# Performance work log

Measured on AMD Instinct MI355X. Metric: run time of the kernel, lower is better.

Reference implementation:

```python
import jax, jax.numpy as jnp
import numpy as np

NUM_COLS = 8      # MyTopoAgent.num_columns
NUM_SELECTED = 4  # MyTopoAgent.num_selected


def _gatv2(x, src, tgt, Wl, bl, Wr, br, att, bias, n):
    """PyG GATv2Conv (share_weights=False, concat=True, negative_slope=0.2).
    x: [n, Din]; src/tgt: [E] (self loops already appended); att: [H, C]."""
    H, C = att.shape
    xl = (x @ Wl + bl).reshape(n, H, C)   # lin_l(x) -> source transform
    xr = (x @ Wr + br).reshape(n, H, C)   # lin_r(x) -> target transform
    # e_ij = att . leaky_relu(xl[j] + xr[i])  per head
    e = jnp.einsum('ehc,hc->eh', jax.nn.leaky_relu(xl[src] + xr[tgt], 0.2), att)  # [E, H]
    # segment softmax over edges sharing a target node (stable via segment max)
    m = jax.lax.stop_gradient(jax.ops.segment_max(e, tgt, num_segments=n))
    ex = jnp.exp(e - m[tgt])
    denom = jax.ops.segment_sum(ex, tgt, num_segments=n)
    alpha = ex / (denom[tgt] + 1e-16)
    out = jax.ops.segment_sum(xl[src] * alpha[..., None], tgt, num_segments=n)  # [n, H, C]
    return out.reshape(n, H * C) + bias


def setup_inputs() -> dict:
    key = jax.random.key(0)
    B, N, D, Hd, Ch, E = 4, 10000, 128, 128, 7, 640000
    M = B * N
    ks = iter(jax.random.split(key, 40))
    nx = lambda shape: jax.random.normal(next(ks), shape, dtype=jnp.float32) * 0.05
    inp = {}
    inp['x'] = jax.random.normal(next(ks), (B, N, D), dtype=jnp.float32)
    inp['edge_index'] = jax.random.randint(next(ks), (2, E), 0, M)
    inp['gumbel_u'] = jax.random.uniform(next(ks), (B, NUM_COLS, Ch), dtype=jnp.float32,
                                         minval=1e-6, maxval=1.0 - 1e-6)
    # actor gat1(D->Hd), actor gat2(Hd->Ch), critic gat1(D->Hd), critic gat2(Hd->Hd); heads=1
    for pre, di, do in (('a1', D, Hd), ('a2', Hd, Ch), ('c1', D, Hd), ('c2', Hd, Hd)):
        inp[pre + '_Wl'] = nx((di, do))
        inp[pre + '_bl'] = jnp.zeros((do,), jnp.float32)
        inp[pre + '_Wr'] = nx((di, do))
        inp[pre + '_br'] = jnp.zeros((do,), jnp.float32)
        inp[pre + '_att'] = nx((1, do))
        inp[pre + '_b'] = jnp.zeros((do,), jnp.float32)
    inp['fc_W'] = nx((Hd, 1))
    inp['fc_b'] = jnp.zeros((1,), jnp.float32)
    return inp


def reference(x, edge_index, gumbel_u,
              a1_Wl, a1_bl, a1_Wr, a1_br, a1_att, a1_b,
              a2_Wl, a2_bl, a2_Wr, a2_br, a2_att, a2_b,
              c1_Wl, c1_bl, c1_Wr, c1_br, c1_att, c1_b,
              c2_Wl, c2_bl, c2_Wr, c2_br, c2_att, c2_b,
              fc_W, fc_b):
    B, N, D = x.shape
    M = B * N
    xf = x.reshape(M, D)
    loops = jnp.arange(M, dtype=edge_index.dtype)  # PyG add_self_loops
    src = jnp.concatenate([edge_index[0], loops])
    tgt = jnp.concatenate([edge_index[1], loops])
    # ---- actor: GATv2 -> leaky_relu(0.01) -> GATv2 -> softmax ----
    h = _gatv2(xf, src, tgt, a1_Wl, a1_bl, a1_Wr, a1_br, a1_att, a1_b, M)
    h = jax.nn.leaky_relu(h, 0.01)
    logits = _gatv2(h, src, tgt, a2_Wl, a2_bl, a2_Wr, a2_br, a2_att, a2_b, M).reshape(B, N, -1)
    probs = jax.nn.softmax(logits, axis=-1)  # [B, N, 7]
    # multinomial(k=4, no replacement) per column via Gumbel top-k
    g = -jnp.log(-jnp.log(gumbel_u))                       # [B, 8, 7]
    scores = jnp.log(probs[:, :NUM_COLS, :]) + g
    _, action = jax.lax.top_k(scores, NUM_SELECTED)        # [B, 8, 4]
    # torch gather(dim=1): sel[b,i,j] = probs[b, action[b,i,j], j]
    sel = probs[jnp.arange(B)[:, None, None], action, jnp.arange(NUM_SELECTED)[None, None, :]]
    # ---- critic: GATv2 -> leaky_relu(0.01) -> GATv2 -> Linear ----
    hc = _gatv2(xf, src, tgt, c1_Wl, c1_bl, c1_Wr, c1_br, c1_att, c1_b, M)
    hc = jax.nn.leaky_relu(hc, 0.01)
    hc = _gatv2(hc, src, tgt, c2_Wl, c2_bl, c2_Wr, c2_br, c2_att, c2_b, M).reshape(B, N, -1)
    value = hc @ fc_W + fc_b  # [B, N, 1]
    return action, sel, value
```

## Files before the change

kernel.cpp:

```cpp
#include <hip/hip_runtime.h>
#include <math.h>


typedef __attribute__((ext_vector_type(8))) short bf16x8;
typedef __attribute__((ext_vector_type(4))) float f32x4;

__device__ __forceinline__ float wave_reduce_sum(float v){
  #pragma unroll
  for (int o = 32; o > 0; o >>= 1) v += __shfl_xor(v, o);
  return v;
}
__device__ __forceinline__ unsigned short f2bf(float f){
  unsigned int u = __float_as_uint(f);
  u += 0x7FFFu + ((u >> 16) & 1u);
  return (unsigned short)(u >> 16);
}
__device__ __forceinline__ void unpack2(unsigned int u, float& a, float& b){
  a = __uint_as_float(u << 16);
  b = __uint_as_float(u & 0xffff0000u);
}

__global__ void k_init(int* __restrict__ p, int nz,
                       const float* __restrict__ W1l, const float* __restrict__ W1r,
                       const float* __restrict__ W2l, const float* __restrict__ W2r,
                       unsigned short* __restrict__ Wt1, unsigned short* __restrict__ Wt2){
  int i = blockIdx.x * blockDim.x + threadIdx.x;
  if (i < nz){
    p[i] = 0;
  } else {
    int r = i - nz;
    if (r < 65536){
      int which = r >> 15;
      int lin = r & 32767;
      const float* Wl = which ? W2l : W1l;
      const float* Wr = which ? W2r : W1r;
      unsigned short* Wt = which ? Wt2 : Wt1;
      int n = lin >> 7, k = lin & 127;
      float v = (n < 128) ? Wl[(size_t)k * 128 + n] : Wr[(size_t)k * 128 + (n - 128)];
      Wt[lin] = f2bf(v);
    }
  }
}

__global__ void k_scatter(const int* __restrict__ ei, int E,
                          int* __restrict__ cnt, int* __restrict__ bucket){
  int e = blockIdx.x * blockDim.x + threadIdx.x;
  if (e >= E) return;
  int s = ei[e], t = ei[E + e];
  int pos = atomicAdd(&cnt[t], 1);
  if (pos < 64) bucket[(size_t)t * 64 + pos] = s;
}

__device__ __forceinline__ void dev_mark1(
    const int* __restrict__ cnt, const int* __restrict__ bucket,
    int* __restrict__ flag1, int* __restrict__ list1, int* __restrict__ n1, int N){
  int p = threadIdx.x;
  if (p >= 32) return;
  int node = (p >> 3) * N + (p & 7);
  if (atomicExch(&flag1[node], 1) == 0) list1[atomicAdd(n1, 1)] = node;
  int deg = min(cnt[node], 64);
  const int* crow = bucket + (size_t)node * 64;
  for (int j = 0; j < deg; ++j){
    int s = crow[j];
    if (atomicExch(&flag1[s], 1) == 0) list1[atomicAdd(n1, 1)] = s;
  }
}
__device__ __forceinline__ void dev_mark2(
    int vbid, int nblk,
    const int* __restrict__ cnt, const int* __restrict__ bucket,
    const int* __restrict__ list1, const int* __restrict__ n1,
    int* __restrict__ flag2, int* __restrict__ list2, int* __restrict__ n2){
  int n = *n1;
  for (int i = vbid * blockDim.x + threadIdx.x; i < n; i += nblk * blockDim.x){
    int node = list1[i];
    if (atomicExch(&flag2[node], 1) == 0) list2[atomicAdd(n2, 1)] = node;
    int deg = min(cnt[node], 64);
    const int* crow = bucket + (size_t)node * 64;
    for (int j = 0; j < deg; ++j){
      int s = crow[j];
      if (atomicExch(&flag2[s], 1) == 0) list2[atomicAdd(n2, 1)] = s;
    }
  }
}

__device__ __forceinline__ void dev_gemm_dual(
    int bid, const float* __restrict__ A,
    const float* __restrict__ Wl, const float* __restrict__ Wr,
    const float* __restrict__ blv, const float* __restrict__ brv,
    float* __restrict__ XL1, float* __restrict__ XR1,
    const int* __restrict__ list1, const int* __restrict__ list2,
    const int* __restrict__ nn,
    float (*As)[17], float (*Ws)[64]){
  const float* W; const float* bias; float* Out; const int* rows; int n;
  int colBase, bx, nbx;
  if (bid < 384){
    W = Wl; bias = blv; Out = XL1; rows = list2; n = nn[1];
    colBase = (bid / 192) * 64; bx = bid % 192; nbx = 192;
  } else {
    int rem = bid - 384;
    W = Wr; bias = brv; Out = XR1; rows = list1; n = nn[0];
    colBase = (rem / 64) * 64; bx = rem % 64; nbx = 64;
  }
  int tid = threadIdx.x;
  int tx = tid & 15, ty = tid >> 4;
  int ar = tid >> 2, ac = (tid & 3) << 2;
  int kr = tid >> 4, nc = (tid & 15) << 2;
  for (int base = bx * 64; base < n; base += nbx * 64){
    float acc[4][4] = {};
    int arow = rows[min(base + ar, n - 1)];
    for (int k0 = 0; k0 < 128; k0 += 16){
      float4 av = *(const float4*)(A + (size_t)arow * 128 + k0 + ac);
      As[ar][ac + 0] = av.x; As[ar][ac + 1] = av.y;
      As[ar][ac + 2] = av.z; As[ar][ac + 3] = av.w;
      float4 wv = *(const float4*)(W + (size_t)(k0 + kr) * 128 + colBase + nc);
      *(float4*)&Ws[kr][nc] = wv;
      __syncthreads();
      #pragma unroll
      for (int kk = 0; kk < 16; ++kk){
        float a0 = As[ty * 4 + 0][kk];
        float a1 = As[ty * 4 + 1][kk];
        float a2 = As[ty * 4 + 2][kk];
        float a3 = As[ty * 4 + 3][kk];
        float4 b = *(const float4*)&Ws[kk][tx * 4];
        acc[0][0] += a0 * b.x; acc[0][1] += a0 * b.y; acc[0][2] += a0 * b.z; acc[0][3] += a0 * b.w;
        acc[1][0] += a1 * b.x; acc[1][1] += a1 * b.y; acc[1][2] += a1 * b.z; acc[1][3] += a1 * b.w;
        acc[2][0] += a2 * b.x; acc[2][1] += a2 * b.y; acc[2][2] += a2 * b.z; acc[2][3] += a2 * b.w;
        acc[3][0] += a3 * b.x; acc[3][1] += a3 * b.y; acc[3][2] += a3 * b.z; acc[3][3] += a3 * b.w;
      }
      __syncthreads();
    }
    int cN = colBase + tx * 4;
    float4 bb = *(const float4*)(bias + cN);
    #pragma unroll
    for (int i = 0; i < 4; ++i){
      int r = rows[min(base + ty * 4 + i, n - 1)];
      float4 o;
      o.x = acc[i][0] + bb.x; o.y = acc[i][1] + bb.y;
      o.z = acc[i][2] + bb.z; o.w = acc[i][3] + bb.w;
      *(float4*)(Out + (size_t)r * 128 + cN) = o;
    }
  }
}

template<bool CVT>
__device__ __forceinline__ void dev_gemm_mfma(
    int rblk, const void* __restrict__ Av, const unsigned short* __restrict__ Wt,
    const float* __restrict__ bl, const float* __restrict__ br,
    unsigned short* __restrict__ XL, unsigned short* __restrict__ XR){
  int w = threadIdx.x >> 6, lane = threadIdx.x & 63;
  int l16 = lane & 15, kg = lane >> 4;
  int rBase = rblk * 64 + w * 16;
  f32x4 acc[16];
  #pragma unroll
  for (int i = 0; i < 16; ++i) acc[i] = (f32x4){0.f, 0.f, 0.f, 0.f};
  #pragma unroll
  for (int ks = 0; ks < 4; ++ks){
    bf16x8 a;
    if constexpr (CVT){
      const float* A = (const float*)Av;
      const float* ap = A + (size_t)(rBase + l16) * 128 + ks * 32 + kg * 8;
      float4 f0 = *(const float4*)ap;
      float4 f1 = *(const float4*)(ap + 4);
      union { bf16x8 v; unsigned short s[8]; } u;
      u.s[0] = f2bf(f0.x); u.s[1] = f2bf(f0.y); u.s[2] = f2bf(f0.z); u.s[3] = f2bf(f0.w);
      u.s[4] = f2bf(f1.x); u.s[5] = f2bf(f1.y); u.s[6] = f2bf(f1.z); u.s[7] = f2bf(f1.w);
      a = u.v;
    } else {
      a = *(const bf16x8*)((const unsigned short*)Av + (size_t)(rBase + l16) * 128 + ks * 32 + kg * 8);
    }
    #pragma unroll
    for (int ct = 0; ct < 16; ++ct){
      bf16x8 wv = *(const bf16x8*)(Wt + (size_t)(ct * 16 + l16) * 128 + ks * 32 + kg * 8);
      acc[ct] = __builtin_amdgcn_mfma_f32_16x16x32_bf16(wv, a, acc[ct], 0, 0, 0);
    }
  }
  int row = rBase + l16;
  #pragma unroll
  for (int ct = 0; ct < 16; ++ct){
    int col = ct * 16 + kg * 4;
    const float* bp = (col < 128) ? (bl + col) : (br + (col - 128));
    float4 bb = *(const float4*)bp;
    unsigned int p0 = (unsigned int)f2bf(acc[ct][0] + bb.x) |
                      ((unsigned int)f2bf(acc[ct][1] + bb.y) << 16);
    unsigned int p1 = (unsigned int)f2bf(acc[ct][2] + bb.z) |
                      ((unsigned int)f2bf(acc[ct][3] + bb.w) << 16);
    unsigned short* dst = (col < 128) ? (XL + (size_t)row * 128 + col)
                                      : (XR + (size_t)row * 128 + (col - 128));
    uint2 pk; pk.x = p0; pk.y = p1;
    *(uint2*)dst = pk;
  }
}

template<int MODE>
__device__ __forceinline__ void dev_gather16(
    int gid, int l,
    const unsigned short* __restrict__ XL, const unsigned short* __restrict__ XR,
    const int* __restrict__ cnt, const int* __restrict__ bucket,
    const float* __restrict__ att, const float* __restrict__ bias,
    const float* __restrict__ fcW, const float* __restrict__ fcb,
    void* __restrict__ outp){
  uint4 xu = *(const uint4*)(XR + (size_t)gid * 128 + l * 8);
  float xr[8];
  unpack2(xu.x, xr[0], xr[1]); unpack2(xu.y, xr[2], xr[3]);
  unpack2(xu.z, xr[4], xr[5]); unpack2(xu.w, xr[6], xr[7]);
  float at[8];
  {
    float4 a0 = *(const float4*)(att + l * 8);
    float4 a1 = *(const float4*)(att + l * 8 + 4);
    at[0] = a0.x; at[1] = a0.y; at[2] = a0.z; at[3] = a0.w;
    at[4] = a1.x; at[5] = a1.y; at[6] = a1.z; at[7] = a1.w;
  }
  int deg = min(cnt[gid], 64);
  const int* __restrict__ crow = bucket + (size_t)gid * 64;
  float m = -INFINITY, den = 0.f;
  float acc[8] = {0.f, 0.f, 0.f, 0.f, 0.f, 0.f, 0.f, 0.f};

  auto proc = [&](uint4 u){
    float xl[8];
    unpack2(u.x, xl[0], xl[1]); unpack2(u.y, xl[2], xl[3]);
    unpack2(u.z, xl[4], xl[5]); unpack2(u.w, xl[6], xl[7]);
    float e = 0.f;
    #pragma unroll
    for (int c = 0; c < 8; ++c){
      float v = xl[c] + xr[c];
      v = fmaxf(v, 0.2f * v);
      e = fmaf(v, at[c], e);
    }
    e += __shfl_xor(e, 1, 16);
    e += __shfl_xor(e, 2, 16);
    e += __shfl_xor(e, 4, 16);
    e += __shfl_xor(e, 8, 16);
    if (e > m){
      float sc = __expf(m - e);
      den *= sc;
      #pragma unroll
      for (int c = 0; c < 8; ++c) acc[c] *= sc;
      m = e;
    }
    float p = __expf(e - m);
    den += p;
    #pragma unroll
    for (int c = 0; c < 8; ++c) acc[c] = fmaf(p, xl[c], acc[c]);
  };

  proc(*(const uint4*)(XL + (size_t)gid * 128 + l * 8));

  int nq = deg >> 2;
  int j = 0;
  if (nq > 0){
    uint4 r0, r1, r2, r3;
    {
      int s0 = crow[0], s1 = crow[1], s2 = crow[2], s3 = crow[3];
      r0 = *(const uint4*)(XL + (size_t)s0 * 128 + l * 8);
      r1 = *(const uint4*)(XL + (size_t)s1 * 128 + l * 8);
      r2 = *(const uint4*)(XL + (size_t)s2 * 128 + l * 8);
      r3 = *(const uint4*)(XL + (size_t)s3 * 128 + l * 8);
    }
    for (int q = 1;; ++q){
      bool more = (q < nq);
      uint4 n0, n1, n2, n3;
      if (more){
        int b4 = q * 4;
        int t0 = crow[b4 + 0], t1 = crow[b4 + 1], t2 = crow[b4 + 2], t3 = crow[b4 + 3];
        n0 = *(const uint4*)(XL + (size_t)t0 * 128 + l * 8);
        n1 = *(const uint4*)(XL + (size_t)t1 * 128 + l * 8);
        n2 = *(const uint4*)(XL + (size_t)t2 * 128 + l * 8);
        n3 = *(const uint4*)(XL + (size_t)t3 * 128 + l * 8);
      }
      proc(r0); proc(r1); proc(r2); proc(r3);
      if (!more) break;
      r0 = n0; r1 = n1; r2 = n2; r3 = n3;
    }
    j = nq * 4;
  }
  for (; j < deg; ++j){
    int s = crow[j];
    proc(*(const uint4*)(XL + (size_t)s * 128 + l * 8));
  }

  float r = 1.f / (den + 1e-16f);
  float4 b0 = *(const float4*)(bias + l * 8);
  float4 b1 = *(const float4*)(bias + l * 8 + 4);
  float o[8];
  o[0] = acc[0] * r + b0.x; o[1] = acc[1] * r + b0.y;
  o[2] = acc[2] * r + b0.z; o[3] = acc[3] * r + b0.w;
  o[4] = acc[4] * r + b1.x; o[5] = acc[5] * r + b1.y;
  o[6] = acc[6] * r + b1.z; o[7] = acc[7] * r + b1.w;
  if (MODE == 0){
    #pragma unroll
    for (int c = 0; c < 8; ++c) o[c] = o[c] > 0.f ? o[c] : 0.01f * o[c];
    uint4 pk;
    pk.x = (unsigned int)f2bf(o[0]) | ((unsigned int)f2bf(o[1]) << 16);
    pk.y = (unsigned int)f2bf(o[2]) | ((unsigned int)f2bf(o[3]) << 16);
    pk.z = (unsigned int)f2bf(o[4]) | ((unsigned int)f2bf(o[5]) << 16);
    pk.w = (unsigned int)f2bf(o[6]) | ((unsigned int)f2bf(o[7]) << 16);
    *(uint4*)((unsigned short*)outp + (size_t)gid * 128 + l * 8) = pk;
  } else {
    float4 w0 = *(const float4*)(fcW + l * 8);
    float4 w1 = *(const float4*)(fcW + l * 8 + 4);
    float pv = o[0] * w0.x + o[1] * w0.y + o[2] * w0.z + o[3] * w0.w +
               o[4] * w1.x + o[5] * w1.y + o[6] * w1.z + o[7] * w1.w;
    pv += __shfl_xor(pv, 1, 16);
    pv += __shfl_xor(pv, 2, 16);
    pv += __shfl_xor(pv, 4, 16);
    pv += __shfl_xor(pv, 8, 16);
    if (l == 0) ((float*)outp)[gid] = pv + fcb[0];
  }
}

__device__ __forceinline__ void dev_a1_fused(
    int vbid,
    const float* __restrict__ XL, const float* __restrict__ XR,
    const int* __restrict__ cnt, const int* __restrict__ bucket,
    const float* __restrict__ att, const float* __restrict__ bias,
    const float* __restrict__ Wl7, const float* __restrict__ Wr7,
    const float* __restrict__ bl7, const float* __restrict__ br7,
    float* __restrict__ XL2, float* __restrict__ XR2,
    const int* __restrict__ list, const int* __restrict__ n_dev){
  int n = *n_dev;
  int lane = threadIdx.x & 63;
  const int wstride = (256 * 256) >> 6;
  for (int i = (vbid * 256 + (int)threadIdx.x) >> 6; i < n; i += wstride){
    int wid = list[i];
    float2 xr = ((const float2*)(XR + (size_t)wid * 128))[lane];
    float2 at = ((const float2*)att)[lane];
    int deg = min(cnt[wid], 64);
    const int* crow = bucket + (size_t)wid * 64;
    float m = -INFINITY, den = 0.f, acc0 = 0.f, acc1 = 0.f;
    for (int j = -1; j < deg; ++j){
      int s = (j < 0) ? wid : crow[j];
      float2 xl = ((const float2*)(XL + (size_t)s * 128))[lane];
      float v0 = xl.x + xr.x, v1 = xl.y + xr.y;
      v0 = v0 > 0.f ? v0 : 0.2f * v0;
      v1 = v1 > 0.f ? v1 : 0.2f * v1;
      float e = wave_reduce_sum(v0 * at.x + v1 * at.y);
      float mn = fmaxf(m, e);
      float sc = __expf(m - mn);
      float p  = __expf(e - mn);
      den  = den  * sc + p;
      acc0 = acc0 * sc + p * xl.x;
      acc1 = acc1 * sc + p * xl.y;
      m = mn;
    }
    float r = 1.f / (den + 1e-16f);
    float2 bs = ((const float2*)bias)[lane];
    float o0 = acc0 * r + bs.x;
    float o1 = acc1 * r + bs.y;
    o0 = o0 > 0.f ? o0 : 0.01f * o0;
    o1 = o1 > 0.f ? o1 : 0.01f * o1;
    #pragma unroll
    for (int c = 0; c < 7; ++c){
      float wl0 = Wl7[(size_t)(2 * lane) * 7 + c];
      float wl1 = Wl7[(size_t)(2 * lane + 1) * 7 + c];
      float wr0 = Wr7[(size_t)(2 * lane) * 7 + c];
      float wr1 = Wr7[(size_t)(2 * lane + 1) * 7 + c];
      float dl = wave_reduce_sum(o0 * wl0 + o1 * wl1);
      float dr = wave_reduce_sum(o0 * wr0 + o1 * wr1);
      if (lane == 0){
        XL2[(size_t)wid * 8 + c] = dl + bl7[c];
        XR2[(size_t)wid * 8 + c] = dr + br7[c];
      }
    }
  }
}

__global__ __launch_bounds__(256) void k_L3(
    const float* __restrict__ x, const unsigned short* __restrict__ Wt1,
    const float* __restrict__ c1_bl, const float* __restrict__ c1_br,
    unsigned short* __restrict__ XLb, unsigned short* __restrict__ XRb, int nMfma,
    const int* __restrict__ cnt, const int* __restrict__ bucket,
    int* __restrict__ flag1, int* __restrict__ list1, int* __restrict__ n1, int N){
  int bid = blockIdx.x;
  if (bid < nMfma){
    dev_gemm_mfma<true>(bid, x, Wt1, c1_bl, c1_br, XLb, XRb);
  } else {
    dev_mark1(cnt, bucket, flag1, list1, n1, N);
  }
}

__global__ __launch_bounds__(256) void k_L4(
    const int* __restrict__ cnt, const int* __restrict__ bucket,
    const int* __restrict__ list1, const int* __restrict__ n1,
    int* __restrict__ flag2, int* __restrict__ list2, int* __restrict__ n2,
    const unsigned short* __restrict__ XLb, const unsigned short* __restrict__ XRb,
    const float* __restrict__ c1_att, const float* __restrict__ c1_b,
    unsigned short* __restrict__ Hb, int M){
  int bid = blockIdx.x;
  if (bid < 64){
    dev_mark2(bid, 64, cnt, bucket, list1, n1, flag2, list2, n2);
  } else {
    int gbid = bid - 64;
    int gid = (gbid * 256 + (int)threadIdx.x) >> 4;
    int l = threadIdx.x & 15;
    if (gid < M)
      dev_gather16<0>(gid, l, XLb, XRb, cnt, bucket, c1_att, c1_b,
                      nullptr, nullptr, (void*)Hb);
  }
}

__global__ __launch_bounds__(256) void k_L5(
    const float* __restrict__ x,
    const float* __restrict__ a1_Wl, const float* __restrict__ a1_Wr,
    const float* __restrict__ a1_bl, const float* __restrict__ a1_br,
    float* __restrict__ XL1, float* __restrict__ XR1,
    const int* __restrict__ list1, const int* __restrict__ list2,
    const int* __restrict__ nn,
    const unsigned short* __restrict__ Hb, const unsigned short* __restrict__ Wt2,
    const float* __restrict__ c2_bl, const float* __restrict__ c2_br,
    unsigned short* __restrict__ XLb, unsigned short* __restrict__ XRb){
  __shared__ float As[64][17];
  __shared__ float Ws[16][64];
  int bid = blockIdx.x;
  if (bid < 512){
    dev_gemm_dual(bid, x, a1_Wl, a1_Wr, a1_bl, a1_br, XL1, XR1, list1, list2, nn, As, Ws);
  } else {
    dev_gemm_mfma<false>(bid - 512, Hb, Wt2, c2_bl, c2_br, XLb, XRb);
  }
}

__global__ __launch_bounds__(256) void k_L6(
    const float* __restrict__ XL1, const float* __restrict__ XR1,
    const int* __restrict__ cnt, const int* __restrict__ bucket,
    const float* __restrict__ a1_att, const float* __restrict__ a1_b,
    const float* __restrict__ Wl7, const float* __restrict__ Wr7,
    const float* __restrict__ bl7, const float* __restrict__ br7,
    float* __restrict__ XL2, float* __restrict__ XR2,
    const int* __restrict__ list1, const int* __restrict__ n1,
    const unsigned short* __restrict__ XLb, const unsigned short* __restrict__ XRb,
    const float* __restrict__ c2_att, const float* __restrict__ c2_b,
    const float* __restrict__ fcW, const float* __restrict__ fcb,
    float* __restrict__ out_value, int M){
  int bid = blockIdx.x;
  if (bid < 256){
    dev_a1_fused(bid, XL1, XR1, cnt, bucket, a1_att, a1_b,
                 Wl7, Wr7, bl7, br7, XL2, XR2, list1, n1);
  } else {
    int gbid = bid - 256;
    int gid = (gbid * 256 + (int)threadIdx.x) >> 4;
    int l = threadIdx.x & 15;
    if (gid < M)
      dev_gather16<1>(gid, l, XLb, XRb, cnt, bucket, c2_att, c2_b,
                      fcW, fcb, (void*)out_value);
  }
}

__global__ __launch_bounds__(256) void k_a2head(
    const float* __restrict__ XL2, const float* __restrict__ XR2,
    const int* __restrict__ cnt, const int* __restrict__ bucket,
    const float* __restrict__ att, const float* __restrict__ bias,
    const float* __restrict__ gu,
    float* __restrict__ out_action, float* __restrict__ out_sel, int N){
  __shared__ float pr[32][8];
  int g = threadIdx.x >> 3, c = threadIdx.x & 7;
  int node = (g >> 3) * N + (g & 7);
  float xr = (c < 7) ? XR2[(size_t)node * 8 + c] : 0.f;
  float at = (c < 7) ? att[c] : 0.f;
  int deg = min(cnt[node], 64);
  const int* crow = bucket + (size_t)node * 64;
  float m = -INFINITY, den = 0.f, acc = 0.f;
  for (int j = -1; j < deg; ++j){
    int s = (j < 0) ? node : crow[j];
    float xl = (c < 7) ? XL2[(size_t)s * 8 + c] : 0.f;
    float v = xl + xr;
    v = fmaxf(v, 0.2f * v);
    float e = v * at;
    e += __shfl_xor(e, 1, 8);
    e += __shfl_xor(e, 2, 8);
    e += __shfl_xor(e, 4, 8);
    if (e > m){
      float sc = __expf(m - e);
      den *= sc; acc *= sc; m = e;
    }
    float p = __expf(e - m);
    den += p;
    acc = fmaf(p, xl, acc);
  }
  float lg = acc / (den + 1e-16f) + ((c < 7) ? bias[c] : 0.f);
  float lgv = (c < 7) ? lg : -INFINITY;
  float mx = lgv;
  mx = fmaxf(mx, __shfl_xor(mx, 1, 8));
  mx = fmaxf(mx, __shfl_xor(mx, 2, 8));
  mx = fmaxf(mx, __shfl_xor(mx, 4, 8));
  float ex = (c < 7) ? expf(lgv - mx) : 0.f;
  float sm = ex;
  sm += __shfl_xor(sm, 1, 8);
  sm += __shfl_xor(sm, 2, 8);
  sm += __shfl_xor(sm, 4, 8);
  pr[g][c] = ex / sm;
  __syncthreads();
  int t = threadIdx.x;
  if (t < 32){
    int b = t >> 3;
    float sc[7];
    #pragma unroll
    for (int cc = 0; cc < 7; ++cc){
      float u = gu[t * 7 + cc];
      float gn = -logf(-logf(u));
      sc[cc] = logf(pr[t][cc]) + gn;
    }
    #pragma unroll
    for (int k = 0; k < 4; ++k){
      float best = -INFINITY; int bi = 0;
      #pragma unroll
      for (int cc = 0; cc < 7; ++cc) if (sc[cc] > best){ best = sc[cc]; bi = cc; }
      sc[bi] = -INFINITY;
      out_action[t * 4 + k] = (float)bi;
      out_sel[t * 4 + k] = pr[b * 8 + bi][k];
    }
  }
}

extern "C" void kernel_launch(void* const* d_in, const int* in_sizes, int n_in,
                              void* d_out, int out_size, void* d_ws, size_t ws_size,
                              hipStream_t stream){
  const float* x  = (const float*)d_in[0];
  const int*   ei = (const int*)d_in[1];
  const float* gu = (const float*)d_in[2];
  const float* a1_Wl = (const float*)d_in[3],  *a1_bl = (const float*)d_in[4];
  const float* a1_Wr = (const float*)d_in[5],  *a1_br = (const float*)d_in[6];
  const float* a1_att= (const float*)d_in[7],  *a1_b  = (const float*)d_in[8];
  const float* a2_Wl = (const float*)d_in[9],  *a2_bl = (const float*)d_in[10];
  const float* a2_Wr = (const float*)d_in[11], *a2_br = (const float*)d_in[12];
  const float* a2_att= (const float*)d_in[13], *a2_b  = (const float*)d_in[14];
  const float* c1_Wl = (const float*)d_in[15], *c1_bl = (const float*)d_in[16];
  const float* c1_Wr = (const float*)d_in[17], *c1_br = (const float*)d_in[18];
  const float* c1_att= (const float*)d_in[19], *c1_b  = (const float*)d_in[20];
  const float* c2_Wl = (const float*)d_in[21], *c2_bl = (const float*)d_in[22];
  const float* c2_Wr = (const float*)d_in[23], *c2_br = (const float*)d_in[24];
  const float* c2_att= (const float*)d_in[25], *c2_b  = (const float*)d_in[26];
  const float* fc_W  = (const float*)d_in[27], *fc_b  = (const float*)d_in[28];

  const int M = in_sizes[0] / 128;
  const int E = in_sizes[1] / 2;
  const int B = in_sizes[2] / 56;
  const int N = M / B;
  const int nw = B * 8;
  const int T = 256;

  char* ws = (char*)d_ws;
  size_t off = 0;
  auto alloc = [&](size_t bytes) -> void* {
    void* p = ws + off;
    off += (bytes + 255) & ~(size_t)255;
    return p;
  };
  int*   cnt    = (int*)alloc((size_t)(3 * M + 2) * 4);
  int*   flag1  = cnt + M;
  int*   flag2  = flag1 + M;
  int*   nn     = flag2 + M;
  int*   bucket = (int*)alloc((size_t)M * 64 * 4);
  int*   list1  = (int*)alloc((size_t)M * 4);
  int*   list2  = (int*)alloc((size_t)M * 4);
  float* XL2    = (float*)alloc((size_t)M * 8 * 4);
  float* XR2    = (float*)alloc((size_t)M * 8 * 4);
  unsigned short* Wt1 = (unsigned short*)alloc((size_t)256 * 128 * 2);
  unsigned short* Wt2 = (unsigned short*)alloc((size_t)256 * 128 * 2);
  float* XL1 = (float*)alloc((size_t)M * 128 * 4);
  float* XR1 = (float*)alloc((size_t)M * 128 * 4);
  unsigned short* XLb = (unsigned short*)alloc((size_t)M * 128 * 2);
  unsigned short* XRb = (unsigned short*)alloc((size_t)M * 128 * 2);
  unsigned short* Hb  = (unsigned short*)alloc((size_t)M * 128 * 2);
  (void)ws_size; (void)n_in; (void)out_size;

  float* out_action = (float*)d_out;
  float* out_sel    = out_action + (size_t)nw * 4;
  float* out_value  = out_sel + (size_t)nw * 4;

  const int G0 = (M * 16 + T - 1) / T;
  const int nMfma = M / 64;
  const int nz = 3 * M + 2;

  k_init<<<(nz + 65536 + T - 1) / T, T, 0, stream>>>(cnt, nz,
      c1_Wl, c1_Wr, c2_Wl, c2_Wr, Wt1, Wt2);
  k_scatter<<<(E + T - 1) / T, T, 0, stream>>>(ei, E, cnt, bucket);
  k_L3<<<nMfma + 1, T, 0, stream>>>(x, Wt1, c1_bl, c1_br, XLb, XRb, nMfma,
      cnt, bucket, flag1, list1, &nn[0], N);
  k_L4<<<64 + G0, T, 0, stream>>>(cnt, bucket, list1, &nn[0], flag2, list2, &nn[1],
      XLb, XRb, c1_att, c1_b, Hb, M);
  k_L5<<<512 + nMfma, T, 0, stream>>>(x, a1_Wl, a1_Wr, a1_bl, a1_br,
      XL1, XR1, list1, list2, nn, Hb, Wt2, c2_bl, c2_br, XLb, XRb);
  k_L6<<<256 + G0, T, 0, stream>>>(XL1, XR1, cnt, bucket, a1_att, a1_b,
      a2_Wl, a2_Wr, a2_bl, a2_br, XL2, XR2, list1, &nn[0],
      XLb, XRb, c2_att, c2_b, fc_W, fc_b, out_value, M);
  k_a2head<<<1, 256, 0, stream>>>(XL2, XR2, cnt, bucket, a2_att, a2_b, gu,
      out_action, out_sel, N);
}
```

Measured before the change: 207.6 us.

## Store edge buckets as 16-bit indices and fold the actor head into k_L6

```diff
diff --git a/kernel.cpp b/kernel.cpp
--- a/kernel.cpp
+++ b/kernel.cpp
@@ -43,23 +43,23 @@
 }
 
 __global__ void k_scatter(const int* __restrict__ ei, int E,
-                          int* __restrict__ cnt, int* __restrict__ bucket){
+                          int* __restrict__ cnt, unsigned short* __restrict__ bucket){
   int e = blockIdx.x * blockDim.x + threadIdx.x;
   if (e >= E) return;
   int s = ei[e], t = ei[E + e];
   int pos = atomicAdd(&cnt[t], 1);
-  if (pos < 64) bucket[(size_t)t * 64 + pos] = s;
+  if (pos < 64) bucket[(size_t)t * 64 + pos] = (unsigned short)s;
 }
 
 __device__ __forceinline__ void dev_mark1(
-    const int* __restrict__ cnt, const int* __restrict__ bucket,
+    const int* __restrict__ cnt, const unsigned short* __restrict__ bucket,
     int* __restrict__ flag1, int* __restrict__ list1, int* __restrict__ n1, int N){
   int p = threadIdx.x;
   if (p >= 32) return;
   int node = (p >> 3) * N + (p & 7);
   if (atomicExch(&flag1[node], 1) == 0) list1[atomicAdd(n1, 1)] = node;
   int deg = min(cnt[node], 64);
-  const int* crow = bucket + (size_t)node * 64;
+  const unsigned short* crow = bucket + (size_t)node * 64;
   for (int j = 0; j < deg; ++j){
     int s = crow[j];
     if (atomicExch(&flag1[s], 1) == 0) list1[atomicAdd(n1, 1)] = s;
@@ -67,7 +67,7 @@
 }
 __device__ __forceinline__ void dev_mark2(
     int vbid, int nblk,
-    const int* __restrict__ cnt, const int* __restrict__ bucket,
+    const int* __restrict__ cnt, const unsigned short* __restrict__ bucket,
     const int* __restrict__ list1, const int* __restrict__ n1,
     int* __restrict__ flag2, int* __restrict__ list2, int* __restrict__ n2){
   int n = *n1;
@@ -75,7 +75,7 @@
     int node = list1[i];
     if (atomicExch(&flag2[node], 1) == 0) list2[atomicAdd(n2, 1)] = node;
     int deg = min(cnt[node], 64);
-    const int* crow = bucket + (size_t)node * 64;
+    const unsigned short* crow = bucket + (size_t)node * 64;
     for (int j = 0; j < deg; ++j){
       int s = crow[j];
       if (atomicExch(&flag2[s], 1) == 0) list2[atomicAdd(n2, 1)] = s;
@@ -195,7 +195,7 @@
 __device__ __forceinline__ void dev_gather16(
     int gid, int l,
     const unsigned short* __restrict__ XL, const unsigned short* __restrict__ XR,
-    const int* __restrict__ cnt, const int* __restrict__ bucket,
+    const int* __restrict__ cnt, const unsigned short* __restrict__ bucket,
     const float* __restrict__ att, const float* __restrict__ bias,
     const float* __restrict__ fcW, const float* __restrict__ fcb,
     void* __restrict__ outp){
@@ -211,7 +211,7 @@
     at[4] = a1.x; at[5] = a1.y; at[6] = a1.z; at[7] = a1.w;
   }
   int deg = min(cnt[gid], 64);
-  const int* __restrict__ crow = bucket + (size_t)gid * 64;
+  const unsigned short* __restrict__ crow = bucket + (size_t)gid * 64;
   float m = -INFINITY, den = 0.f;
   float acc[8] = {0.f, 0.f, 0.f, 0.f, 0.f, 0.f, 0.f, 0.f};
 
@@ -311,7 +311,7 @@
 __device__ __forceinline__ void dev_a1_fused(
     int vbid,
     const float* __restrict__ XL, const float* __restrict__ XR,
-    const int* __restrict__ cnt, const int* __restrict__ bucket,
+    const int* __restrict__ cnt, const unsigned short* __restrict__ bucket,
     const float* __restrict__ att, const float* __restrict__ bias,
     const float* __restrict__ Wl7, const float* __restrict__ Wr7,
     const float* __restrict__ bl7, const float* __restrict__ br7,
@@ -325,7 +325,7 @@
     float2 xr = ((const float2*)(XR + (size_t)wid * 128))[lane];
     float2 at = ((const float2*)att)[lane];
     int deg = min(cnt[wid], 64);
-    const int* crow = bucket + (size_t)wid * 64;
+    const unsigned short* crow = bucket + (size_t)wid * 64;
     float m = -INFINITY, den = 0.f, acc0 = 0.f, acc1 = 0.f;
     for (int j = -1; j < deg; ++j){
       int s = (j < 0) ? wid : crow[j];
@@ -364,11 +364,77 @@
   }
 }
 
+__device__ __forceinline__ void dev_a2head(
+    float (*pr)[8],
+    const float* __restrict__ XL2, const float* __restrict__ XR2,
+    const int* __restrict__ cnt, const unsigned short* __restrict__ bucket,
+    const float* __restrict__ att, const float* __restrict__ bias,
+    const float* __restrict__ gu,
+    float* __restrict__ out_action, float* __restrict__ out_sel, int N){
+  int g = threadIdx.x >> 3, c = threadIdx.x & 7;
+  int node = (g >> 3) * N + (g & 7);
+  float xr = (c < 7) ? XR2[(size_t)node * 8 + c] : 0.f;
+  float at = (c < 7) ? att[c] : 0.f;
+  int deg = min(cnt[node], 64);
+  const unsigned short* crow = bucket + (size_t)node * 64;
+  float m = -INFINITY, den = 0.f, acc = 0.f;
+  for (int j = -1; j < deg; ++j){
+    int s = (j < 0) ? node : crow[j];
+    float xl = (c < 7) ? XL2[(size_t)s * 8 + c] : 0.f;
+    float v = xl + xr;
+    v = fmaxf(v, 0.2f * v);
+    float e = v * at;
+    e += __shfl_xor(e, 1, 8);
+    e += __shfl_xor(e, 2, 8);
+    e += __shfl_xor(e, 4, 8);
+    if (e > m){
+      float sc = __expf(m - e);
+      den *= sc; acc *= sc; m = e;
+    }
+    float p = __expf(e - m);
+    den += p;
+    acc = fmaf(p, xl, acc);
+  }
+  float lg = acc / (den + 1e-16f) + ((c < 7) ? bias[c] : 0.f);
+  float lgv = (c < 7) ? lg : -INFINITY;
+  float mx = lgv;
+  mx = fmaxf(mx, __shfl_xor(mx, 1, 8));
+  mx = fmaxf(mx, __shfl_xor(mx, 2, 8));
+  mx = fmaxf(mx, __shfl_xor(mx, 4, 8));
+  float ex = (c < 7) ? expf(lgv - mx) : 0.f;
+  float sm = ex;
+  sm += __shfl_xor(sm, 1, 8);
+  sm += __shfl_xor(sm, 2, 8);
+  sm += __shfl_xor(sm, 4, 8);
+  pr[g][c] = ex / sm;
+  __syncthreads();
+  int t = threadIdx.x;
+  if (t < 32){
+    int b = t >> 3;
+    float sc[7];
+    #pragma unroll
+    for (int cc = 0; cc < 7; ++cc){
+      float u = gu[t * 7 + cc];
+      float gn = -logf(-logf(u));
+      sc[cc] = logf(pr[t][cc]) + gn;
+    }
+    #pragma unroll
+    for (int k = 0; k < 4; ++k){
+      float best = -INFINITY; int bi = 0;
+      #pragma unroll
+      for (int cc = 0; cc < 7; ++cc) if (sc[cc] > best){ best = sc[cc]; bi = cc; }
+      sc[bi] = -INFINITY;
+      out_action[t * 4 + k] = (float)bi;
+      out_sel[t * 4 + k] = pr[b * 8 + bi][k];
+    }
+  }
+}
+
 __global__ __launch_bounds__(256) void k_L3(
     const float* __restrict__ x, const unsigned short* __restrict__ Wt1,
     const float* __restrict__ c1_bl, const float* __restrict__ c1_br,
     unsigned short* __restrict__ XLb, unsigned short* __restrict__ XRb, int nMfma,
-    const int* __restrict__ cnt, const int* __restrict__ bucket,
+    const int* __restrict__ cnt, const unsigned short* __restrict__ bucket,
     int* __restrict__ flag1, int* __restrict__ list1, int* __restrict__ n1, int N){
   int bid = blockIdx.x;
   if (bid < nMfma){
@@ -379,7 +445,7 @@
 }
 
 __global__ __launch_bounds__(256) void k_L4(
-    const int* __restrict__ cnt, const int* __restrict__ bucket,
+    const int* __restrict__ cnt, const unsigned short* __restrict__ bucket,
     const int* __restrict__ list1, const int* __restrict__ n1,
     int* __restrict__ flag2, int* __restrict__ list2, int* __restrict__ n2,
     const unsigned short* __restrict__ XLb, const unsigned short* __restrict__ XRb,
@@ -420,20 +486,38 @@
 
 __global__ __launch_bounds__(256) void k_L6(
     const float* __restrict__ XL1, const float* __restrict__ XR1,
-    const int* __restrict__ cnt, const int* __restrict__ bucket,
+    const int* __restrict__ cnt, const unsigned short* __restrict__ bucket,
     const float* __restrict__ a1_att, const float* __restrict__ a1_b,
     const float* __restrict__ Wl7, const float* __restrict__ Wr7,
     const float* __restrict__ bl7, const float* __restrict__ br7,
     float* __restrict__ XL2, float* __restrict__ XR2,
     const int* __restrict__ list1, const int* __restrict__ n1,
+    int* __restrict__ done,
+    const float* __restrict__ a2_att, const float* __restrict__ a2_b,
+    const float* __restrict__ gu,
+    float* __restrict__ out_action, float* __restrict__ out_sel, int N,
     const unsigned short* __restrict__ XLb, const unsigned short* __restrict__ XRb,
     const float* __restrict__ c2_att, const float* __restrict__ c2_b,
     const float* __restrict__ fcW, const float* __restrict__ fcb,
     float* __restrict__ out_value, int M){
+  __shared__ float pr[32][8];
+  __shared__ int isLast;
   int bid = blockIdx.x;
   if (bid < 256){
     dev_a1_fused(bid, XL1, XR1, cnt, bucket, a1_att, a1_b,
                  Wl7, Wr7, bl7, br7, XL2, XR2, list1, n1);
+    __syncthreads();
+    if (threadIdx.x == 0){
+      __threadfence();
+      int v = atomicAdd(done, 1);
+      isLast = (v == 255);
+    }
+    __syncthreads();
+    if (isLast){
+      __threadfence();
+      dev_a2head(pr, XL2, XR2, cnt, bucket, a2_att, a2_b, gu,
+                 out_action, out_sel, N);
+    }
   } else {
     int gbid = bid - 256;
     int gid = (gbid * 256 + (int)threadIdx.x) >> 4;
@@ -441,72 +525,6 @@
     if (gid < M)
       dev_gather16<1>(gid, l, XLb, XRb, cnt, bucket, c2_att, c2_b,
                       fcW, fcb, (void*)out_value);
-  }
-}
-
-__global__ __launch_bounds__(256) void k_a2head(
-    const float* __restrict__ XL2, const float* __restrict__ XR2,
-    const int* __restrict__ cnt, const int* __restrict__ bucket,
-    const float* __restrict__ att, const float* __restrict__ bias,
-    const float* __restrict__ gu,
-    float* __restrict__ out_action, float* __restrict__ out_sel, int N){
-  __shared__ float pr[32][8];
-  int g = threadIdx.x >> 3, c = threadIdx.x & 7;
-  int node = (g >> 3) * N + (g & 7);
-  float xr = (c < 7) ? XR2[(size_t)node * 8 + c] : 0.f;
-  float at = (c < 7) ? att[c] : 0.f;
-  int deg = min(cnt[node], 64);
-  const int* crow = bucket + (size_t)node * 64;
-  float m = -INFINITY, den = 0.f, acc = 0.f;
-  for (int j = -1; j < deg; ++j){
-    int s = (j < 0) ? node : crow[j];
-    float xl = (c < 7) ? XL2[(size_t)s * 8 + c] : 0.f;
-    float v = xl + xr;
-    v = fmaxf(v, 0.2f * v);
-    float e = v * at;
-    e += __shfl_xor(e, 1, 8);
-    e += __shfl_xor(e, 2, 8);
-    e += __shfl_xor(e, 4, 8);
-    if (e > m){
-      float sc = __expf(m - e);
-      den *= sc; acc *= sc; m = e;
-    }
-    float p = __expf(e - m);
-    den += p;
-    acc = fmaf(p, xl, acc);
-  }
-  float lg = acc / (den + 1e-16f) + ((c < 7) ? bias[c] : 0.f);
-  float lgv = (c < 7) ? lg : -INFINITY;
-  float mx = lgv;
-  mx = fmaxf(mx, __shfl_xor(mx, 1, 8));
-  mx = fmaxf(mx, __shfl_xor(mx, 2, 8));
-  mx = fmaxf(mx, __shfl_xor(mx, 4, 8));
-  float ex = (c < 7) ? expf(lgv - mx) : 0.f;
-  float sm = ex;
-  sm += __shfl_xor(sm, 1, 8);
-  sm += __shfl_xor(sm, 2, 8);
-  sm += __shfl_xor(sm, 4, 8);
-  pr[g][c] = ex / sm;
-  __syncthreads();
-  int t = threadIdx.x;
-  if (t < 32){
-    int b = t >> 3;
-    float sc[7];
-    #pragma unroll
-    for (int cc = 0; cc < 7; ++cc){
-      float u = gu[t * 7 + cc];
-      float gn = -logf(-logf(u));
-      sc[cc] = logf(pr[t][cc]) + gn;
-    }
-    #pragma unroll
-    for (int k = 0; k < 4; ++k){
-      float best = -INFINITY; int bi = 0;
-      #pragma unroll
-      for (int cc = 0; cc < 7; ++cc) if (sc[cc] > best){ best = sc[cc]; bi = cc; }
-      sc[bi] = -INFINITY;
-      out_action[t * 4 + k] = (float)bi;
-      out_sel[t * 4 + k] = pr[b * 8 + bi][k];
-    }
   }
 }
 
@@ -544,11 +562,11 @@
     off += (bytes + 255) & ~(size_t)255;
     return p;
   };
-  int*   cnt    = (int*)alloc((size_t)(3 * M + 2) * 4);
+  int*   cnt    = (int*)alloc((size_t)(3 * M + 4) * 4);
   int*   flag1  = cnt + M;
   int*   flag2  = flag1 + M;
   int*   nn     = flag2 + M;
-  int*   bucket = (int*)alloc((size_t)M * 64 * 4);
+  unsigned short* bucket = (unsigned short*)alloc((size_t)M * 64 * 2);
   int*   list1  = (int*)alloc((size_t)M * 4);
   int*   list2  = (int*)alloc((size_t)M * 4);
   float* XL2    = (float*)alloc((size_t)M * 8 * 4);
@@ -568,7 +586,7 @@
 
   const int G0 = (M * 16 + T - 1) / T;
   const int nMfma = M / 64;
-  const int nz = 3 * M + 2;
+  const int nz = 3 * M + 4;
 
   k_init<<<(nz + 65536 + T - 1) / T, T, 0, stream>>>(cnt, nz,
       c1_Wl, c1_Wr, c2_Wl, c2_Wr, Wt1, Wt2);
@@ -580,8 +598,7 @@
   k_L5<<<512 + nMfma, T, 0, stream>>>(x, a1_Wl, a1_Wr, a1_bl, a1_br,
       XL1, XR1, list1, list2, nn, Hb, Wt2, c2_bl, c2_br, XLb, XRb);
   k_L6<<<256 + G0, T, 0, stream>>>(XL1, XR1, cnt, bucket, a1_att, a1_b,
-      a2_Wl, a2_Wr, a2_bl, a2_br, XL2, XR2, list1, &nn[0],
+      a2_Wl, a2_Wr, a2_bl, a2_br, XL2, XR2, list1, &nn[0], &nn[2],
+      a2_att, a2_b, gu, out_action, out_sel, N,
       XLb, XRb, c2_att, c2_b, fc_W, fc_b, out_value, M);
-  k_a2head<<<1, 256, 0, stream>>>(XL2, XR2, cnt, bucket, a2_att, a2_b, gu,
-      out_action, out_sel, N);
-}
+}
```

Measured after the change: 206.2 us. No clear change (-0.7%).
